# Kernel optimization log

Measured on AMD Instinct MI355X. Metric: run time of the kernel, lower is better.

The kernel has to match this reference:

```python
import jax, jax.numpy as jnp
import numpy as np

N_NODES = 50000
N_EDGES = 800000
N_TRAIN = 40000
IN_DIM = 129  # node_dim + encoding_dim


def _gatv2(x, src, dst, Wl, Wr, att, bias, heads, out_ch, n_nodes):
    """PyG GATv2Conv (share_weights=False, concat=True, aggr='mean', eval mode).
    x: [N, F_in]; src/dst: [E]; Wl/Wr: [F_in, heads*out_ch]; att: [heads, out_ch]."""
    xl = (x @ Wl).reshape(-1, heads, out_ch)          # source transform  [N,H,C]
    xr = (x @ Wr).reshape(-1, heads, out_ch)          # target transform  [N,H,C]
    e = jax.nn.leaky_relu(xl[src] + xr[dst], 0.2)     # [E,H,C]
    logits = jnp.einsum('ehc,hc->eh', e, att)         # [E,H]
    # segment softmax over incoming edges of each target node
    m = jax.ops.segment_max(logits, dst, num_segments=n_nodes)   # [N,H]
    a = jnp.exp(logits - m[dst])
    denom = jax.ops.segment_sum(a, dst, num_segments=n_nodes)    # [N,H]
    alpha = a / denom[dst]                                       # [E,H]
    msg = xl[src] * alpha[:, :, None]                            # [E,H,C]
    summed = jax.ops.segment_sum(msg, dst, num_segments=n_nodes) # [N,H,C]
    deg = jax.ops.segment_sum(jnp.ones((src.shape[0],), x.dtype), dst,
                              num_segments=n_nodes)              # aggr='mean'
    out = summed / jnp.maximum(deg, 1.0)[:, None, None]
    return out.reshape(n_nodes, heads * out_ch) + bias


def setup_inputs() -> dict:
    key = jax.random.key(0)
    ks = jax.random.split(key, 16)
    x = jax.random.normal(ks[0], (N_NODES, IN_DIM), jnp.float32)
    edge_index = jax.random.randint(ks[1], (2, N_EDGES), 0, N_NODES, jnp.int64)
    y = jax.random.uniform(ks[2], (N_NODES,), jnp.float32)
    train_idx = jnp.sort(jax.random.randint(ks[3], (N_TRAIN,), 0, N_NODES, jnp.int64))

    def lin(k, fi, fo):
        return jax.random.normal(k, (fi, fo), jnp.float32) * (1.0 / np.sqrt(fi))

    return {
        'x': x, 'edge_index': edge_index, 'y': y, 'train_idx': train_idx,
        # layer 1: 129 -> 128, heads=2 (concat -> 256)
        'W1l': lin(ks[4], IN_DIM, 256), 'W1r': lin(ks[5], IN_DIM, 256),
        'a1': jax.random.normal(ks[6], (2, 128), jnp.float32) * 0.1,
        'b1': jnp.zeros((256,), jnp.float32),
        # layer 2: 256 -> 128, heads=1
        'W2l': lin(ks[7], 256, 128), 'W2r': lin(ks[8], 256, 128),
        'a2': jax.random.normal(ks[9], (1, 128), jnp.float32) * 0.1,
        'b2': jnp.zeros((128,), jnp.float32),
        # layer 3: 128 -> 1, heads=1
        'W3l': lin(ks[10], 128, 1), 'W3r': lin(ks[11], 128, 1),
        'a3': jax.random.normal(ks[12], (1, 1), jnp.float32) * 0.1,
        'b3': jnp.zeros((1,), jnp.float32),
    }


def reference(x, edge_index, y, train_idx,
              W1l, W1r, a1, b1, W2l, W2r, a2, b2, W3l, W3r, a3, b3):
    src, dst = edge_index[0], edge_index[1]
    n = x.shape[0]
    h = _gatv2(x, src, dst, W1l, W1r, a1, b1, 2, 128, n)   # [N,256]
    h = _gatv2(h, src, dst, W2l, W2r, a2, b2, 1, 128, n)   # [N,128]
    h = _gatv2(h, src, dst, W3l, W3r, a3, b3, 1, 1, n)     # [N,1]
    pred = jax.nn.sigmoid(h.squeeze(-1))                   # [N]
    return pred[train_idx], y[train_idx]
```

## Files before the change

kernel.cpp:

```cpp
#include <hip/hip_runtime.h>
#include <cmath>

__device__ __forceinline__ float lo16(unsigned u){ union{unsigned x; float f;} c; c.x = u << 16; return c.f; }
__device__ __forceinline__ float hi16(unsigned u){ union{unsigned x; float f;} c; c.x = u & 0xffff0000u; return c.f; }
__device__ __forceinline__ float leaky(float v){ return fmaxf(v, 0.2f*v); }
__device__ __forceinline__ unsigned short f2bf(float f){
  union { float f; unsigned u; } c; c.f = f;
  unsigned u = c.u + 0x7FFFu + ((c.u >> 16) & 1u);
  return (unsigned short)(u >> 16);
}
__device__ __forceinline__ unsigned pack2bf(float a, float b){
  return (unsigned)f2bf(a) | ((unsigned)f2bf(b) << 16);
}
__device__ __forceinline__ float mergef(float m, float M){ return (m == M) ? 1.f : __expf(m - M); }

typedef __attribute__((ext_vector_type(8))) short bfrag;
typedef __attribute__((ext_vector_type(4))) float ffrag;


__global__ void deg_kernel(const int* __restrict__ dst, int* __restrict__ degi, int E){
  int e = blockIdx.x*256 + threadIdx.x;
  if (e < E) atomicAdd(&degi[dst[e]], 1);
}

__global__ void scan_p1(const int* __restrict__ degi, int* __restrict__ bsum, int N){
  __shared__ int red[256];
  int t = threadIdx.x;
  int i = blockIdx.x*256 + t;
  red[t] = (i < N) ? degi[i] : 0;
  __syncthreads();
  for (int off = 128; off > 0; off >>= 1){
    if (t < off) red[t] += red[t + off];
    __syncthreads();
  }
  if (t == 0) bsum[blockIdx.x] = red[0];
}

__global__ void scan_p2(const int* __restrict__ bsum, int* __restrict__ boff,
                        int* __restrict__ row_off, int NB, int N){
  __shared__ int s[256];
  int t = threadIdx.x;
  int v = (t < NB) ? bsum[t] : 0;
  s[t] = v;
  __syncthreads();
  for (int off = 1; off < 256; off <<= 1){
    int q = (t >= off) ? s[t - off] : 0;
    __syncthreads();
    s[t] += q;
    __syncthreads();
  }
  if (t < NB) boff[t] = s[t] - v;
  if (t == NB-1) row_off[N] = s[t];
}

__global__ void scan_p3(const int* __restrict__ degi, const int* __restrict__ boff,
                        int* __restrict__ row_off, int N){
  __shared__ int s[256];
  int t = threadIdx.x;
  int i = blockIdx.x*256 + t;
  int v = (i < N) ? degi[i] : 0;
  s[t] = v;
  __syncthreads();
  for (int off = 1; off < 256; off <<= 1){
    int q = (t >= off) ? s[t - off] : 0;
    __syncthreads();
    s[t] += q;
    __syncthreads();
  }
  if (i < N) row_off[i] = boff[blockIdx.x] + s[t] - v;
}

__global__ void scatter_kernel(const int* __restrict__ src, const int* __restrict__ dst,
                               const int* __restrict__ row_off, int* __restrict__ cursor,
                               int* __restrict__ csr_src, int E){
  int e = blockIdx.x*256 + threadIdx.x;
  if (e < E){
    int d = dst[e];
    int pos = row_off[d] + atomicAdd(&cursor[d], 1);
    csr_src[pos] = src[e];
  }
}


__global__ void prep_all(const float* __restrict__ x,
                         const float* __restrict__ W1l, const float* __restrict__ W1r,
                         const float* __restrict__ W2l, const float* __restrict__ W2r,
                         unsigned short* __restrict__ Xbf,
                         unsigned short* __restrict__ WT1,
                         unsigned short* __restrict__ WT2, int N){
  int idx = blockIdx.x*256 + threadIdx.x;
  int n1 = N*160;
  int n2 = 2*256*160;
  int n3 = 2*128*256;
  if (idx < n1){
    int n = idx / 160, k = idx - n*160;
    Xbf[idx] = (k < 129) ? f2bf(x[(size_t)n*129 + k]) : (unsigned short)0;
  } else if (idx < n1 + n2){
    int j = idx - n1;
    int c = j / 160, k = j - c*160;
    float v = 0.f;
    if (k < 129) v = (c < 256) ? W1l[(size_t)k*256 + c] : W1r[(size_t)k*256 + (c - 256)];
    WT1[j] = f2bf(v);
  } else if (idx < n1 + n2 + n3){
    int j = idx - n1 - n2;
    int c = j >> 8, k = j & 255;
    float v = (c < 128) ? W2l[(size_t)k*128 + c] : W2r[(size_t)k*128 + (c - 128)];
    WT2[j] = f2bf(v);
  }
}


template<int CB>
__global__ __launch_bounds__(256) void gemm_dual(const unsigned short* __restrict__ Xbf,
                                                 const unsigned short* __restrict__ WT,
                                                 unsigned short* __restrict__ outBF,
                                                 float* __restrict__ outF,
                                                 int N, int Kpad, int Mhalf){
  __shared__ __attribute__((aligned(16))) unsigned short Xs[128*40];
  __shared__ __attribute__((aligned(16))) unsigned short Ws[CB*128*40];
  int t = threadIdx.x;
  int n0 = blockIdx.x*128, c0 = blockIdx.y*(CB*128);
  int wv = t >> 6, lane = t & 63;
  int wr = wv >> 1, wc = wv & 1;
  int m16 = lane & 15, quad = lane >> 4;

  ffrag acc[CB][4][4];
  #pragma unroll
  for (int cb = 0; cb < CB; cb++)
    #pragma unroll
    for (int i = 0; i < 4; i++)
      #pragma unroll
      for (int j = 0; j < 4; j++) acc[cb][i][j] = (ffrag){0.f,0.f,0.f,0.f};

  for (int k0 = 0; k0 < Kpad; k0 += 32){
    uint4 zero = {0,0,0,0};
    #pragma unroll
    for (int it = 0; it < 2; it++){
      int idx = t + it*256;
      int r = idx >> 2, g = idx & 3;
      int n = n0 + r;
      uint4 v = (n < N) ? *(const uint4*)&Xbf[(size_t)n*Kpad + k0 + g*8] : zero;
      *(uint4*)&Xs[r*40 + g*8] = v;
    }
    #pragma unroll
    for (int it = 0; it < 2*CB; it++){
      int idx = t + it*256;
      int c = idx >> 2, g = idx & 3;
      uint4 v = *(const uint4*)&WT[(size_t)(c0 + c)*Kpad + k0 + g*8];
      *(uint4*)&Ws[c*40 + g*8] = v;
    }
    __syncthreads();
    bfrag a[4];
    #pragma unroll
    for (int i = 0; i < 4; i++)
      a[i] = *(const bfrag*)&Xs[(wr*64 + i*16 + m16)*40 + quad*8];
    #pragma unroll
    for (int cb = 0; cb < CB; cb++){
      bfrag b[4];
      #pragma unroll
      for (int j = 0; j < 4; j++)
        b[j] = *(const bfrag*)&Ws[(cb*128 + wc*64 + j*16 + m16)*40 + quad*8];
      #pragma unroll
      for (int i = 0; i < 4; i++)
        #pragma unroll
        for (int j = 0; j < 4; j++)
          acc[cb][i][j] = __builtin_amdgcn_mfma_f32_16x16x32_bf16(a[i], b[j], acc[cb][i][j], 0, 0, 0);
    }
    __syncthreads();
  }

  #pragma unroll
  for (int cb = 0; cb < CB; cb++){
    int gc0 = c0 + cb*128;
    bool isBF = (gc0 < Mhalf);
    int ccol0 = isBF ? gc0 : (gc0 - Mhalf);
    #pragma unroll
    for (int i = 0; i < 4; i++){
      #pragma unroll
      for (int reg = 0; reg < 4; reg++){
        int rr = n0 + wr*64 + i*16 + quad*4 + reg;
        if (rr >= N) continue;
        #pragma unroll
        for (int j = 0; j < 4; j++){
          int cc = ccol0 + wc*64 + j*16 + m16;
          float v = acc[cb][i][j][reg];
          if (isBF) outBF[(size_t)rr*Mhalf + cc] = f2bf(v);
          else      outF [(size_t)rr*Mhalf + cc] = v;
        }
      }
    }
  }
}


__global__ __launch_bounds__(256) void fused_gat_wave2(
    const int* __restrict__ row_off, const int* __restrict__ csr_src,
    const unsigned short* __restrict__ xlbf, const float* __restrict__ xr,
    const float* __restrict__ att, const float* __restrict__ bias,
    unsigned short* __restrict__ outbf, int N)
{
  int n = blockIdx.x*4 + (threadIdx.x >> 6);
  if (n >= N) return;
  int lane = threadIdx.x & 63;
  int slot = lane >> 5;
  int sub  = lane & 31;
  int ch0  = sub*8;
  int r0 = row_off[n], r1 = row_off[n+1];
  int deg = r1 - r0;

  const float4* xrp = (const float4*)(xr + (size_t)n*256 + ch0);
  float4 xra = xrp[0], xrb = xrp[1];
  const float4* atp = (const float4*)(att + ch0);
  float4 ata = atp[0], atb = atp[1];

  float m = -INFINITY, l = 0.f;
  float a0=0.f,a1=0.f,a2=0.f,a3=0.f,a4=0.f,a5=0.f,a6=0.f,a7=0.f;

  if (deg > 0){
    int p = r0 + slot;
    int pc = min(p, r1-1);
    uint4 cur = *(const uint4*)&xlbf[(size_t)csr_src[pc]*256 + ch0];
    for (; p < r1; p += 2){
      int pn = min(p+2, r1-1);
      uint4 nxt = *(const uint4*)&xlbf[(size_t)csr_src[pn]*256 + ch0];
      float x0=lo16(cur.x), x1=hi16(cur.x), x2=lo16(cur.y), x3=hi16(cur.y);
      float x4=lo16(cur.z), x5=hi16(cur.z), x6=lo16(cur.w), x7=hi16(cur.w);
      float dot = leaky(x0+xra.x)*ata.x + leaky(x1+xra.y)*ata.y
                + leaky(x2+xra.z)*ata.z + leaky(x3+xra.w)*ata.w
                + leaky(x4+xrb.x)*atb.x + leaky(x5+xrb.y)*atb.y
                + leaky(x6+xrb.z)*atb.z + leaky(x7+xrb.w)*atb.w;
      dot += __shfl_xor(dot, 8);
      dot += __shfl_xor(dot, 4);
      dot += __shfl_xor(dot, 2);
      dot += __shfl_xor(dot, 1);
      if (dot <= m){
        float w_ = __expf(dot - m);
        l += w_;
        a0 += w_*x0; a1 += w_*x1; a2 += w_*x2; a3 += w_*x3;
        a4 += w_*x4; a5 += w_*x5; a6 += w_*x6; a7 += w_*x7;
      } else {
        float sc = __expf(m - dot);
        l = l*sc + 1.f;
        a0 = a0*sc + x0; a1 = a1*sc + x1; a2 = a2*sc + x2; a3 = a3*sc + x3;
        a4 = a4*sc + x4; a5 = a5*sc + x5; a6 = a6*sc + x6; a7 = a7*sc + x7;
        m = dot;
      }
      cur = nxt;
    }
  }

  const float4* bvp = (const float4*)(bias + ch0);
  float4 res0 = bvp[0], res1 = bvp[1];
  if (deg > 0){
    float m2 = __shfl_xor(m, 32);
    float l2 = __shfl_xor(l, 32);
    float M  = fmaxf(m, m2);
    float fa = mergef(m, M), fb = mergef(m2, M);
    float L  = l*fa + l2*fb;
    float q;
    q = __shfl_xor(a0,32); a0 = a0*fa + q*fb;
    q = __shfl_xor(a1,32); a1 = a1*fa + q*fb;
    q = __shfl_xor(a2,32); a2 = a2*fa + q*fb;
    q = __shfl_xor(a3,32); a3 = a3*fa + q*fb;
    q = __shfl_xor(a4,32); a4 = a4*fa + q*fb;
    q = __shfl_xor(a5,32); a5 = a5*fa + q*fb;
    q = __shfl_xor(a6,32); a6 = a6*fa + q*fb;
    q = __shfl_xor(a7,32); a7 = a7*fa + q*fb;
    float inv = 1.f / (L * (float)deg);
    res0.x += a0*inv; res0.y += a1*inv; res0.z += a2*inv; res0.w += a3*inv;
    res1.x += a4*inv; res1.y += a5*inv; res1.z += a6*inv; res1.w += a7*inv;
  }
  if (slot == 0){
    uint4 u;
    u.x = pack2bf(res0.x, res0.y);
    u.y = pack2bf(res0.z, res0.w);
    u.z = pack2bf(res1.x, res1.y);
    u.w = pack2bf(res1.z, res1.w);
    *(uint4*)&outbf[(size_t)n*256 + ch0] = u;
  }
}


__global__ __launch_bounds__(256) void fused_gat_wave1(
    const int* __restrict__ row_off, const int* __restrict__ csr_src,
    const unsigned short* __restrict__ xlbf, const float* __restrict__ xr,
    const float* __restrict__ att, const float* __restrict__ bias,
    float* __restrict__ out, int N)
{
  int n = blockIdx.x*4 + (threadIdx.x >> 6);
  if (n >= N) return;
  int lane = threadIdx.x & 63;
  int slot = lane >> 4;
  int sub  = lane & 15;
  int ch0  = sub*8;
  int r0 = row_off[n], r1 = row_off[n+1];
  int deg = r1 - r0;

  const float4* xrp = (const float4*)(xr + (size_t)n*128 + ch0);
  float4 xra = xrp[0], xrb = xrp[1];
  const float4* atp = (const float4*)(att + ch0);
  float4 ata = atp[0], atb = atp[1];

  float m = -INFINITY, l = 0.f;
  float a0=0.f,a1=0.f,a2=0.f,a3=0.f,a4=0.f,a5=0.f,a6=0.f,a7=0.f;

  if (deg > 0){
    int p = r0 + slot;
    int pc = min(p, r1-1);
    uint4 cur = *(const uint4*)&xlbf[(size_t)csr_src[pc]*128 + ch0];
    for (; p < r1; p += 4){
      int pn = min(p+4, r1-1);
      uint4 nxt = *(const uint4*)&xlbf[(size_t)csr_src[pn]*128 + ch0];
      float x0=lo16(cur.x), x1=hi16(cur.x), x2=lo16(cur.y), x3=hi16(cur.y);
      float x4=lo16(cur.z), x5=hi16(cur.z), x6=lo16(cur.w), x7=hi16(cur.w);
      float dot = leaky(x0+xra.x)*ata.x + leaky(x1+xra.y)*ata.y
                + leaky(x2+xra.z)*ata.z + leaky(x3+xra.w)*ata.w
                + leaky(x4+xrb.x)*atb.x + leaky(x5+xrb.y)*atb.y
                + leaky(x6+xrb.z)*atb.z + leaky(x7+xrb.w)*atb.w;
      dot += __shfl_xor(dot, 8);
      dot += __shfl_xor(dot, 4);
      dot += __shfl_xor(dot, 2);
      dot += __shfl_xor(dot, 1);
      if (dot <= m){
        float w_ = __expf(dot - m);
        l += w_;
        a0 += w_*x0; a1 += w_*x1; a2 += w_*x2; a3 += w_*x3;
        a4 += w_*x4; a5 += w_*x5; a6 += w_*x6; a7 += w_*x7;
      } else {
        float sc = __expf(m - dot);
        l = l*sc + 1.f;
        a0 = a0*sc + x0; a1 = a1*sc + x1; a2 = a2*sc + x2; a3 = a3*sc + x3;
        a4 = a4*sc + x4; a5 = a5*sc + x5; a6 = a6*sc + x6; a7 = a7*sc + x7;
        m = dot;
      }
      cur = nxt;
    }
  }

  const float4* bvp = (const float4*)(bias + ch0);
  float4 res0 = bvp[0], res1 = bvp[1];
  if (deg > 0){
    #pragma unroll
    for (int stage = 0; stage < 2; stage++){
      int d = 16 << stage;
      float m2 = __shfl_xor(m, d);
      float l2 = __shfl_xor(l, d);
      float M  = fmaxf(m, m2);
      float fa = mergef(m, M), fb = mergef(m2, M);
      l = l*fa + l2*fb;
      float q;
      q = __shfl_xor(a0,d); a0 = a0*fa + q*fb;
      q = __shfl_xor(a1,d); a1 = a1*fa + q*fb;
      q = __shfl_xor(a2,d); a2 = a2*fa + q*fb;
      q = __shfl_xor(a3,d); a3 = a3*fa + q*fb;
      q = __shfl_xor(a4,d); a4 = a4*fa + q*fb;
      q = __shfl_xor(a5,d); a5 = a5*fa + q*fb;
      q = __shfl_xor(a6,d); a6 = a6*fa + q*fb;
      q = __shfl_xor(a7,d); a7 = a7*fa + q*fb;
      m = M;
    }
    float inv = 1.f / (l * (float)deg);
    res0.x += a0*inv; res0.y += a1*inv; res0.z += a2*inv; res0.w += a3*inv;
    res1.x += a4*inv; res1.y += a5*inv; res1.z += a6*inv; res1.w += a7*inv;
  }
  if (slot == 0){
    float4* op = (float4*)(out + (size_t)n*128 + ch0);
    op[0] = res0; op[1] = res1;
  }
}


__global__ __launch_bounds__(256) void gemm3_kernel(const float* __restrict__ h2,
                                                    const float* __restrict__ W3l,
                                                    const float* __restrict__ W3r,
                                                    float* __restrict__ xl3,
                                                    float* __restrict__ xr3, int N){
  int n = blockIdx.x*4 + (threadIdx.x >> 6);
  int lane = threadIdx.x & 63;
  if (n >= N) return;
  float v1 = h2[(size_t)n*128 + lane];
  float v2 = h2[(size_t)n*128 + 64 + lane];
  float al = v1*W3l[lane] + v2*W3l[64 + lane];
  float ar = v1*W3r[lane] + v2*W3r[64 + lane];
  #pragma unroll
  for (int off = 32; off > 0; off >>= 1){
    al += __shfl_down(al, off);
    ar += __shfl_down(ar, off);
  }
  if (lane == 0){ xl3[n] = al; xr3[n] = ar; }
}

__global__ __launch_bounds__(256) void aggr3_wave(
    const int* __restrict__ row_off, const int* __restrict__ csr_src,
    const float* __restrict__ xl3, const float* __restrict__ xr3,
    const float* __restrict__ a3, const float* __restrict__ b3,
    float* __restrict__ h3, int N)
{
  int n = blockIdx.x*4 + (threadIdx.x >> 6);
  if (n >= N) return;
  int lane = threadIdx.x & 63;
  int r0 = row_off[n], r1 = row_off[n+1];
  int deg = r1 - r0;
  float b = b3[0];
  if (deg == 0){ if (lane == 0) h3[n] = b; return; }
  float xrv = xr3[n];
  float aa = a3[0];
  float m = -INFINITY, den = 0.f, s = 0.f;
  for (int base = r0; base < r1; base += 64){
    int p = base + lane;
    bool valid = p < r1;
    float xlv = valid ? xl3[csr_src[p]] : 0.f;
    float v = leaky(xlv + xrv) * aa;
    if (!valid) v = -INFINITY;
    float bm = v;
    #pragma unroll
    for (int off = 32; off > 0; off >>= 1) bm = fmaxf(bm, __shfl_xor(bm, off));
    float nm = fmaxf(m, bm);
    float a = valid ? __expf(v - nm) : 0.f;
    float bd = a, bs = a * xlv;
    #pragma unroll
    for (int off = 32; off > 0; off >>= 1){
      bd += __shfl_xor(bd, off);
      bs += __shfl_xor(bs, off);
    }
    float sc = __expf(m - nm);
    den = den*sc + bd;
    s   = s*sc + bs;
    m = nm;
  }
  if (lane == 0) h3[n] = s/den/(float)deg + b;
}

__global__ void out_kernel(const float* __restrict__ h3, const float* __restrict__ y,
                           const int* __restrict__ tidx, float* __restrict__ out, int T){
  int i = blockIdx.x*256 + threadIdx.x;
  if (i >= T) return;
  int n = tidx[i];
  out[i] = 1.f/(1.f + __expf(-h3[n]));
  out[T + i] = y[n];
}


extern "C" void kernel_launch(void* const* d_in, const int* in_sizes, int n_in,
                              void* d_out, int out_size, void* d_ws, size_t ws_size,
                              hipStream_t stream){
  const float* x    = (const float*)d_in[0];
  const int*   ei   = (const int*)d_in[1];
  const float* y    = (const float*)d_in[2];
  const int*   tidx = (const int*)d_in[3];
  const float* W1l  = (const float*)d_in[4];
  const float* W1r  = (const float*)d_in[5];
  const float* a1   = (const float*)d_in[6];
  const float* b1   = (const float*)d_in[7];
  const float* W2l  = (const float*)d_in[8];
  const float* W2r  = (const float*)d_in[9];
  const float* a2   = (const float*)d_in[10];
  const float* b2   = (const float*)d_in[11];
  const float* W3l  = (const float*)d_in[12];
  const float* W3r  = (const float*)d_in[13];
  const float* a3   = (const float*)d_in[14];
  const float* b3   = (const float*)d_in[15];

  int N = in_sizes[2];
  int E = in_sizes[1] / 2;
  int T = in_sizes[3];
  const int* src = ei;
  const int* dst = ei + E;
  int NB = (N + 255) / 256;

  char* w = (char*)d_ws;
  size_t off = 0;
  auto take = [&](size_t bytes) -> char* {
    char* p = w + off;
    off = (off + bytes + 255) & ~(size_t)255;
    return p;
  };
  int*   row_off = (int*)  take((size_t)(N+1)*4);
  int*   degi    = (int*)  take((size_t)N*4);
  int*   cursor  = (int*)  take((size_t)N*4);
  int*   bsum    = (int*)  take((size_t)NB*4);
  int*   boff    = (int*)  take((size_t)NB*4);
  int*   csr_src = (int*)  take((size_t)E*4);
  unsigned short* WT1 = (unsigned short*)take((size_t)512*160*2);
  unsigned short* WT2 = (unsigned short*)take((size_t)256*256*2);
  float* A       = (float*)take((size_t)N*256*4);
  float* B       = (float*)take((size_t)N*256*4);

  hipMemsetAsync(degi, 0, (size_t)N*4, stream);
  hipMemsetAsync(cursor, 0, (size_t)N*4, stream);
  deg_kernel<<<(E+255)/256, 256, 0, stream>>>(dst, degi, E);
  scan_p1<<<NB, 256, 0, stream>>>(degi, bsum, N);
  scan_p2<<<1, 256, 0, stream>>>(bsum, boff, row_off, NB, N);
  scan_p3<<<NB, 256, 0, stream>>>(degi, boff, row_off, N);
  scatter_kernel<<<(E+255)/256, 256, 0, stream>>>(src, dst, row_off, cursor, csr_src, E);

  unsigned short* xl1bf = (unsigned short*)A;
  unsigned short* Xbf   = (unsigned short*)(A + (size_t)N*128);
  float*          xr1   = B;
  int prep_total = N*160 + 2*256*160 + 2*128*256;
  prep_all<<<(prep_total+255)/256, 256, 0, stream>>>(x, W1l, W1r, W2l, W2r, Xbf, WT1, WT2, N);

  unsigned short* h1bf = (unsigned short*)(A + (size_t)N*128);
  gemm_dual<2><<<dim3((N+127)/128, 2), 256, 0, stream>>>(Xbf, WT1, xl1bf, xr1, N, 160, 256);
  fused_gat_wave2<<<(N+3)/4, 256, 0, stream>>>(row_off, csr_src, xl1bf, xr1, a1, b1, h1bf, N);

  unsigned short* xl2bf = (unsigned short*)A;
  float*          xr2   = B;
  gemm_dual<1><<<dim3((N+127)/128, 2), 256, 0, stream>>>(h1bf, WT2, xl2bf, xr2, N, 256, 128);
  fused_gat_wave1<<<(N+3)/4, 256, 0, stream>>>(row_off, csr_src, xl2bf, xr2, a2, b2, xr2, N);
  float* h2 = xr2;

  float* Bu  = B + (size_t)N*128;
  float* xl3 = Bu;
  float* xr3 = Bu + N;
  float* h3  = Bu + 2*(size_t)N;
  gemm3_kernel<<<(N+3)/4, 256, 0, stream>>>(h2, W3l, W3r, xl3, xr3, N);
  aggr3_wave<<<(N+3)/4, 256, 0, stream>>>(row_off, csr_src, xl3, xr3, a3, b3, h3, N);

  out_kernel<<<(T+255)/256, 256, 0, stream>>>(h3, y, tidx, (float*)d_out, T);
}
```

Before: 410.0 us.

## Split leaky-ReLU into linear and abs parts, store xr and h2 in bf16

Rewrites leaky_relu(v) as 0.6*v + 0.4*|v|. The linear part of the attention logit then splits into a per-source dot with att, precomputed by new srcsum kernels, plus a per-target dot computed once per node. The target transforms xr and the layer-2 output h2 are now stored as bf16 instead of fp32, which cuts memory traffic in the aggregation and gemm3 kernels. The layer-2 GEMM now runs with CB=2 on a single column block. The cost is two extra small kernels, one more gather per edge for the source sums, and some precision loss on xr and h2.

```diff
diff --git a/kernel.cpp b/kernel.cpp
--- a/kernel.cpp
+++ b/kernel.cpp
@@ -3,7 +3,6 @@
 
 __device__ __forceinline__ float lo16(unsigned u){ union{unsigned x; float f;} c; c.x = u << 16; return c.f; }
 __device__ __forceinline__ float hi16(unsigned u){ union{unsigned x; float f;} c; c.x = u & 0xffff0000u; return c.f; }
-__device__ __forceinline__ float leaky(float v){ return fmaxf(v, 0.2f*v); }
 __device__ __forceinline__ unsigned short f2bf(float f){
   union { float f; unsigned u; } c; c.f = f;
   unsigned u = c.u + 0x7FFFu + ((c.u >> 16) & 1u);
@@ -113,8 +112,8 @@
 template<int CB>
 __global__ __launch_bounds__(256) void gemm_dual(const unsigned short* __restrict__ Xbf,
                                                  const unsigned short* __restrict__ WT,
-                                                 unsigned short* __restrict__ outBF,
-                                                 float* __restrict__ outF,
+                                                 unsigned short* __restrict__ outL,
+                                                 unsigned short* __restrict__ outR,
                                                  int N, int Kpad, int Mhalf){
   __shared__ __attribute__((aligned(16))) unsigned short Xs[128*40];
   __shared__ __attribute__((aligned(16))) unsigned short Ws[CB*128*40];
@@ -172,8 +171,9 @@
   #pragma unroll
   for (int cb = 0; cb < CB; cb++){
     int gc0 = c0 + cb*128;
-    bool isBF = (gc0 < Mhalf);
-    int ccol0 = isBF ? gc0 : (gc0 - Mhalf);
+    bool isL = (gc0 < Mhalf);
+    unsigned short* outp = isL ? outL : outR;
+    int ccol0 = isL ? gc0 : (gc0 - Mhalf);
     #pragma unroll
     for (int i = 0; i < 4; i++){
       #pragma unroll
@@ -183,9 +183,7 @@
         #pragma unroll
         for (int j = 0; j < 4; j++){
           int cc = ccol0 + wc*64 + j*16 + m16;
-          float v = acc[cb][i][j][reg];
-          if (isBF) outBF[(size_t)rr*Mhalf + cc] = f2bf(v);
-          else      outF [(size_t)rr*Mhalf + cc] = v;
+          outp[(size_t)rr*Mhalf + cc] = f2bf(acc[cb][i][j][reg]);
         }
       }
     }
@@ -193,11 +191,44 @@
 }
 
 
+__global__ __launch_bounds__(256) void srcsum2(const unsigned short* __restrict__ xlbf,
+                                               const float* __restrict__ att,
+                                               float* __restrict__ sxl, int N){
+  int n = blockIdx.x*4 + (threadIdx.x >> 6);
+  if (n >= N) return;
+  int lane = threadIdx.x & 63;
+  int ch0 = lane*4;
+  uint2 u = *(const uint2*)&xlbf[(size_t)n*256 + ch0];
+  float4 a = *(const float4*)(att + ch0);
+  float s = lo16(u.x)*a.x + hi16(u.x)*a.y + lo16(u.y)*a.z + hi16(u.y)*a.w;
+  s += __shfl_xor(s, 16);
+  s += __shfl_xor(s, 8);
+  s += __shfl_xor(s, 4);
+  s += __shfl_xor(s, 2);
+  s += __shfl_xor(s, 1);
+  if ((lane & 31) == 0) sxl[(size_t)n*2 + (lane >> 5)] = s;
+}
+
+__global__ __launch_bounds__(256) void srcsum1(const unsigned short* __restrict__ xlbf,
+                                               const float* __restrict__ att,
+                                               float* __restrict__ sxl, int N){
+  int n = blockIdx.x*4 + (threadIdx.x >> 6);
+  if (n >= N) return;
+  int lane = threadIdx.x & 63;
+  unsigned u = *(const unsigned*)&xlbf[(size_t)n*128 + lane*2];
+  float a0 = att[lane*2], a1 = att[lane*2+1];
+  float s = lo16(u)*a0 + hi16(u)*a1;
+  #pragma unroll
+  for (int off = 32; off > 0; off >>= 1) s += __shfl_xor(s, off);
+  if (lane == 0) sxl[n] = s;
+}
+
+
 __global__ __launch_bounds__(256) void fused_gat_wave2(
     const int* __restrict__ row_off, const int* __restrict__ csr_src,
-    const unsigned short* __restrict__ xlbf, const float* __restrict__ xr,
-    const float* __restrict__ att, const float* __restrict__ bias,
-    unsigned short* __restrict__ outbf, int N)
+    const unsigned short* __restrict__ xlbf, const unsigned short* __restrict__ xrbf,
+    const float2* __restrict__ sxl, const float* __restrict__ att,
+    const float* __restrict__ bias, unsigned short* __restrict__ outbf, int N)
 {
   int n = blockIdx.x*4 + (threadIdx.x >> 6);
   if (n >= N) return;
@@ -208,10 +239,18 @@
   int r0 = row_off[n], r1 = row_off[n+1];
   int deg = r1 - r0;
 
-  const float4* xrp = (const float4*)(xr + (size_t)n*256 + ch0);
-  float4 xra = xrp[0], xrb = xrp[1];
+  uint4 xru = *(const uint4*)&xrbf[(size_t)n*256 + ch0];
+  float q0=lo16(xru.x), q1=hi16(xru.x), q2=lo16(xru.y), q3=hi16(xru.y);
+  float q4=lo16(xru.z), q5=hi16(xru.z), q6=lo16(xru.w), q7=hi16(xru.w);
   const float4* atp = (const float4*)(att + ch0);
   float4 ata = atp[0], atb = atp[1];
+
+  float sxr = q0*ata.x + q1*ata.y + q2*ata.z + q3*ata.w
+            + q4*atb.x + q5*atb.y + q6*atb.z + q7*atb.w;
+  sxr += __shfl_xor(sxr, 8);
+  sxr += __shfl_xor(sxr, 4);
+  sxr += __shfl_xor(sxr, 2);
+  sxr += __shfl_xor(sxr, 1);
 
   float m = -INFINITY, l = 0.f;
   float a0=0.f,a1=0.f,a2=0.f,a3=0.f,a4=0.f,a5=0.f,a6=0.f,a7=0.f;
@@ -219,20 +258,26 @@
   if (deg > 0){
     int p = r0 + slot;
     int pc = min(p, r1-1);
-    uint4 cur = *(const uint4*)&xlbf[(size_t)csr_src[pc]*256 + ch0];
+    int s = csr_src[pc];
+    uint4 cur = *(const uint4*)&xlbf[(size_t)s*256 + ch0];
+    float2 sl = sxl[s];
     for (; p < r1; p += 2){
       int pn = min(p+2, r1-1);
-      uint4 nxt = *(const uint4*)&xlbf[(size_t)csr_src[pn]*256 + ch0];
+      int s2 = csr_src[pn];
+      uint4 nxt = *(const uint4*)&xlbf[(size_t)s2*256 + ch0];
+      float2 sln = sxl[s2];
       float x0=lo16(cur.x), x1=hi16(cur.x), x2=lo16(cur.y), x3=hi16(cur.y);
       float x4=lo16(cur.z), x5=hi16(cur.z), x6=lo16(cur.w), x7=hi16(cur.w);
-      float dot = leaky(x0+xra.x)*ata.x + leaky(x1+xra.y)*ata.y
-                + leaky(x2+xra.z)*ata.z + leaky(x3+xra.w)*ata.w
-                + leaky(x4+xrb.x)*atb.x + leaky(x5+xrb.y)*atb.y
-                + leaky(x6+xrb.z)*atb.z + leaky(x7+xrb.w)*atb.w;
-      dot += __shfl_xor(dot, 8);
-      dot += __shfl_xor(dot, 4);
-      dot += __shfl_xor(dot, 2);
-      dot += __shfl_xor(dot, 1);
+      float ab = fabsf(x0+q0)*ata.x + fabsf(x1+q1)*ata.y
+               + fabsf(x2+q2)*ata.z + fabsf(x3+q3)*ata.w
+               + fabsf(x4+q4)*atb.x + fabsf(x5+q5)*atb.y
+               + fabsf(x6+q6)*atb.z + fabsf(x7+q7)*atb.w;
+      ab += __shfl_xor(ab, 8);
+      ab += __shfl_xor(ab, 4);
+      ab += __shfl_xor(ab, 2);
+      ab += __shfl_xor(ab, 1);
+      float slh = (sub < 16) ? sl.x : sl.y;
+      float dot = 0.6f*(slh + sxr) + 0.4f*ab;
       if (dot <= m){
         float w_ = __expf(dot - m);
         l += w_;
@@ -245,7 +290,7 @@
         a4 = a4*sc + x4; a5 = a5*sc + x5; a6 = a6*sc + x6; a7 = a7*sc + x7;
         m = dot;
       }
-      cur = nxt;
+      cur = nxt; sl = sln;
     }
   }
 
@@ -283,9 +328,9 @@
 
 __global__ __launch_bounds__(256) void fused_gat_wave1(
     const int* __restrict__ row_off, const int* __restrict__ csr_src,
-    const unsigned short* __restrict__ xlbf, const float* __restrict__ xr,
-    const float* __restrict__ att, const float* __restrict__ bias,
-    float* __restrict__ out, int N)
+    const unsigned short* __restrict__ xlbf, const unsigned short* __restrict__ xrbf,
+    const float* __restrict__ sxl, const float* __restrict__ att,
+    const float* __restrict__ bias, unsigned short* __restrict__ outbf, int N)
 {
   int n = blockIdx.x*4 + (threadIdx.x >> 6);
   if (n >= N) return;
@@ -296,10 +341,18 @@
   int r0 = row_off[n], r1 = row_off[n+1];
   int deg = r1 - r0;
 
-  const float4* xrp = (const float4*)(xr + (size_t)n*128 + ch0);
-  float4 xra = xrp[0], xrb = xrp[1];
+  uint4 xru = *(const uint4*)&xrbf[(size_t)n*128 + ch0];
+  float q0=lo16(xru.x), q1=hi16(xru.x), q2=lo16(xru.y), q3=hi16(xru.y);
+  float q4=lo16(xru.z), q5=hi16(xru.z), q6=lo16(xru.w), q7=hi16(xru.w);
   const float4* atp = (const float4*)(att + ch0);
   float4 ata = atp[0], atb = atp[1];
+
+  float sxr = q0*ata.x + q1*ata.y + q2*ata.z + q3*ata.w
+            + q4*atb.x + q5*atb.y + q6*atb.z + q7*atb.w;
+  sxr += __shfl_xor(sxr, 8);
+  sxr += __shfl_xor(sxr, 4);
+  sxr += __shfl_xor(sxr, 2);
+  sxr += __shfl_xor(sxr, 1);
 
   float m = -INFINITY, l = 0.f;
   float a0=0.f,a1=0.f,a2=0.f,a3=0.f,a4=0.f,a5=0.f,a6=0.f,a7=0.f;
@@ -307,20 +360,25 @@
   if (deg > 0){
     int p = r0 + slot;
     int pc = min(p, r1-1);
-    uint4 cur = *(const uint4*)&xlbf[(size_t)csr_src[pc]*128 + ch0];
+    int s = csr_src[pc];
+    uint4 cur = *(const uint4*)&xlbf[(size_t)s*128 + ch0];
+    float sl = sxl[s];
     for (; p < r1; p += 4){
       int pn = min(p+4, r1-1);
-      uint4 nxt = *(const uint4*)&xlbf[(size_t)csr_src[pn]*128 + ch0];
+      int s2 = csr_src[pn];
+      uint4 nxt = *(const uint4*)&xlbf[(size_t)s2*128 + ch0];
+      float sln = sxl[s2];
       float x0=lo16(cur.x), x1=hi16(cur.x), x2=lo16(cur.y), x3=hi16(cur.y);
       float x4=lo16(cur.z), x5=hi16(cur.z), x6=lo16(cur.w), x7=hi16(cur.w);
-      float dot = leaky(x0+xra.x)*ata.x + leaky(x1+xra.y)*ata.y
-                + leaky(x2+xra.z)*ata.z + leaky(x3+xra.w)*ata.w
-                + leaky(x4+xrb.x)*atb.x + leaky(x5+xrb.y)*atb.y
-                + leaky(x6+xrb.z)*atb.z + leaky(x7+xrb.w)*atb.w;
-      dot += __shfl_xor(dot, 8);
-      dot += __shfl_xor(dot, 4);
-      dot += __shfl_xor(dot, 2);
-      dot += __shfl_xor(dot, 1);
+      float ab = fabsf(x0+q0)*ata.x + fabsf(x1+q1)*ata.y
+               + fabsf(x2+q2)*ata.z + fabsf(x3+q3)*ata.w
+               + fabsf(x4+q4)*atb.x + fabsf(x5+q5)*atb.y
+               + fabsf(x6+q6)*atb.z + fabsf(x7+q7)*atb.w;
+      ab += __shfl_xor(ab, 8);
+      ab += __shfl_xor(ab, 4);
+      ab += __shfl_xor(ab, 2);
+      ab += __shfl_xor(ab, 1);
+      float dot = 0.6f*(sl + sxr) + 0.4f*ab;
       if (dot <= m){
         float w_ = __expf(dot - m);
         l += w_;
@@ -333,7 +391,7 @@
         a4 = a4*sc + x4; a5 = a5*sc + x5; a6 = a6*sc + x6; a7 = a7*sc + x7;
         m = dot;
       }
-      cur = nxt;
+      cur = nxt; sl = sln;
     }
   }
 
@@ -364,13 +422,17 @@
     res1.x += a4*inv; res1.y += a5*inv; res1.z += a6*inv; res1.w += a7*inv;
   }
   if (slot == 0){
-    float4* op = (float4*)(out + (size_t)n*128 + ch0);
-    op[0] = res0; op[1] = res1;
-  }
-}
-
-
-__global__ __launch_bounds__(256) void gemm3_kernel(const float* __restrict__ h2,
+    uint4 u;
+    u.x = pack2bf(res0.x, res0.y);
+    u.y = pack2bf(res0.z, res0.w);
+    u.z = pack2bf(res1.x, res1.y);
+    u.w = pack2bf(res1.z, res1.w);
+    *(uint4*)&outbf[(size_t)n*128 + ch0] = u;
+  }
+}
+
+
+__global__ __launch_bounds__(256) void gemm3_kernel(const unsigned short* __restrict__ h2,
                                                     const float* __restrict__ W3l,
                                                     const float* __restrict__ W3r,
                                                     float* __restrict__ xl3,
@@ -378,14 +440,14 @@
   int n = blockIdx.x*4 + (threadIdx.x >> 6);
   int lane = threadIdx.x & 63;
   if (n >= N) return;
-  float v1 = h2[(size_t)n*128 + lane];
-  float v2 = h2[(size_t)n*128 + 64 + lane];
-  float al = v1*W3l[lane] + v2*W3l[64 + lane];
-  float ar = v1*W3r[lane] + v2*W3r[64 + lane];
+  unsigned u = *(const unsigned*)&h2[(size_t)n*128 + lane*2];
+  float v1 = lo16(u), v2 = hi16(u);
+  float al = v1*W3l[lane*2] + v2*W3l[lane*2+1];
+  float ar = v1*W3r[lane*2] + v2*W3r[lane*2+1];
   #pragma unroll
   for (int off = 32; off > 0; off >>= 1){
-    al += __shfl_down(al, off);
-    ar += __shfl_down(ar, off);
+    al += __shfl_xor(al, off);
+    ar += __shfl_xor(ar, off);
   }
   if (lane == 0){ xl3[n] = al; xr3[n] = ar; }
 }
@@ -410,7 +472,8 @@
     int p = base + lane;
     bool valid = p < r1;
     float xlv = valid ? xl3[csr_src[p]] : 0.f;
-    float v = leaky(xlv + xrv) * aa;
+    float t = xlv + xrv;
+    float v = fmaxf(t, 0.2f*t) * aa;
     if (!valid) v = -INFINITY;
     float bm = v;
     #pragma unroll
@@ -496,25 +559,32 @@
 
   unsigned short* xl1bf = (unsigned short*)A;
   unsigned short* Xbf   = (unsigned short*)(A + (size_t)N*128);
-  float*          xr1   = B;
+  unsigned short* h1bf  = (unsigned short*)(A + (size_t)N*128);
+  unsigned short* xr1bf = (unsigned short*)B;
+  float* Bu   = B + (size_t)N*128;
+  float* sxl1 = Bu;
+  float* sxl2 = Bu + 2*(size_t)N;
+  float* xl3  = Bu + 4*(size_t)N;
+  float* xr3  = Bu + 5*(size_t)N;
+  float* h3   = Bu + 6*(size_t)N;
+
   int prep_total = N*160 + 2*256*160 + 2*128*256;
   prep_all<<<(prep_total+255)/256, 256, 0, stream>>>(x, W1l, W1r, W2l, W2r, Xbf, WT1, WT2, N);
 
-  unsigned short* h1bf = (unsigned short*)(A + (size_t)N*128);
-  gemm_dual<2><<<dim3((N+127)/128, 2), 256, 0, stream>>>(Xbf, WT1, xl1bf, xr1, N, 160, 256);
-  fused_gat_wave2<<<(N+3)/4, 256, 0, stream>>>(row_off, csr_src, xl1bf, xr1, a1, b1, h1bf, N);
+  gemm_dual<2><<<dim3((N+127)/128, 2), 256, 0, stream>>>(Xbf, WT1, xl1bf, xr1bf, N, 160, 256);
+  srcsum2<<<(N+3)/4, 256, 0, stream>>>(xl1bf, a1, sxl1, N);
+  fused_gat_wave2<<<(N+3)/4, 256, 0, stream>>>(row_off, csr_src, xl1bf, xr1bf,
+                                               (const float2*)sxl1, a1, b1, h1bf, N);
 
   unsigned short* xl2bf = (unsigned short*)A;
-  float*          xr2   = B;
-  gemm_dual<1><<<dim3((N+127)/128, 2), 256, 0, stream>>>(h1bf, WT2, xl2bf, xr2, N, 256, 128);
-  fused_gat_wave1<<<(N+3)/4, 256, 0, stream>>>(row_off, csr_src, xl2bf, xr2, a2, b2, xr2, N);
-  float* h2 = xr2;
-
-  float* Bu  = B + (size_t)N*128;
-  float* xl3 = Bu;
-  float* xr3 = Bu + N;
-  float* h3  = Bu + 2*(size_t)N;
-  gemm3_kernel<<<(N+3)/4, 256, 0, stream>>>(h2, W3l, W3r, xl3, xr3, N);
+  unsigned short* xr2bf = (unsigned short*)B;
+  gemm_dual<2><<<dim3((N+127)/128, 1), 256, 0, stream>>>(h1bf, WT2, xl2bf, xr2bf, N, 256, 128);
+  srcsum1<<<(N+3)/4, 256, 0, stream>>>(xl2bf, a2, sxl2, N);
+  fused_gat_wave1<<<(N+3)/4, 256, 0, stream>>>(row_off, csr_src, xl2bf, xr2bf,
+                                               sxl2, a2, b2, xr2bf, N);
+  unsigned short* h2bf = xr2bf;
+
+  gemm3_kernel<<<(N+3)/4, 256, 0, stream>>>(h2bf, W3l, W3r, xl3, xr3, N);
   aggr3_wave<<<(N+3)/4, 256, 0, stream>>>(row_off, csr_src, xl3, xr3, a3, b3, h3, N);
 
   out_kernel<<<(T+255)/256, 256, 0, stream>>>(h3, y, tidx, (float*)d_out, T);
```

After: 423.3 us. 1.03x slower.
